# Kernel optimization log

Measured on AMD Instinct MI355X. Metric: run time of the kernel, lower is better.

The kernel has to match this reference:

```python
import jax, jax.numpy as jnp
import numpy as np

WAYS, SHOTS = 5, 5
F_DIM, HID = 1024, 512          # num_node_feats, int(1024*0.5)
BATCH = 2048                    # num_tasks
N = WAYS * SHOTS + 1            # 26 samples per episode
BN_EPS = 1e-5


def setup_inputs() -> dict:
    key = jax.random.key(0)
    ks = jax.random.split(key, 12)
    d = {"node_feats": jax.random.normal(ks[0], (BATCH, N, F_DIM), jnp.float32)}
    # conv1 (1x1): F_DIM -> HID, bn1; conv2: HID -> HID, bn2; conv4: HID -> F_DIM
    d["w1"] = jax.random.normal(ks[1], (HID, F_DIM), jnp.float32) * (1.0 / np.sqrt(F_DIM))
    d["b1"] = jax.random.normal(ks[2], (HID,), jnp.float32) * 0.01
    d["g1"] = jnp.ones((HID,), jnp.float32)
    d["be1"] = jnp.zeros((HID,), jnp.float32)
    d["m1"] = jax.random.normal(ks[3], (HID,), jnp.float32) * 0.1
    d["v1"] = jax.random.uniform(ks[4], (HID,), jnp.float32, 0.5, 1.5)
    d["w2"] = jax.random.normal(ks[5], (HID, HID), jnp.float32) * (1.0 / np.sqrt(HID))
    d["b2"] = jax.random.normal(ks[6], (HID,), jnp.float32) * 0.01
    d["g2"] = jnp.ones((HID,), jnp.float32)
    d["be2"] = jnp.zeros((HID,), jnp.float32)
    d["m2"] = jax.random.normal(ks[7], (HID,), jnp.float32) * 0.1
    d["v2"] = jax.random.uniform(ks[8], (HID,), jnp.float32, 0.5, 1.5)
    d["w3"] = jax.random.normal(ks[9], (F_DIM, HID), jnp.float32) * (1.0 / np.sqrt(HID))
    d["b3"] = jax.random.normal(ks[10], (F_DIM,), jnp.float32) * 0.01
    return d


def _conv1x1(x, w, b):
    # x: [B, Cin, N], w: [Cout, Cin] -> [B, Cout, N]
    return jnp.einsum('bcn,oc->bon', x, w) + b[None, :, None]


def _bn(x, g, be, m, v):
    # inference BatchNorm1d over channel dim of [B, C, N]
    scale = g / jnp.sqrt(v + BN_EPS)
    return (x - m[None, :, None]) * scale[None, :, None] + be[None, :, None]


def _forward(node_feats, w1, b1, g1, be1, m1, v1, w2, b2, g2, be2, m2, v2, w3, b3):
    B, n, F = node_feats.shape  # n == WAYS*SHOTS+1
    # in-place per-class mean on the transpose view also mutates node_feats in torch:
    sup = node_feats[:, :WAYS * SHOTS].reshape(B, WAYS, SHOTS, F)
    sup = jnp.broadcast_to(sup.mean(axis=2, keepdims=True), sup.shape).reshape(B, WAYS * SHOTS, F)
    nf = jnp.concatenate([sup, node_feats[:, WAYS * SHOTS:]], axis=1)  # [B, N, F]

    x = nf.transpose(0, 2, 1)  # [B, F, N]
    x = jax.nn.leaky_relu(_bn(_conv1x1(x, w1, b1), g1, be1, m1, v1), 0.01)
    x = jax.nn.leaky_relu(_bn(_conv1x1(x, w2, b2), g2, be2, m2, v2), 0.01)
    att = jax.nn.sigmoid(_conv1x1(x, w3, b3))  # [B, F, N]

    # sim_cal: cosine sim of u_ij = a_i*a_j*x_i vs v_ij = a_i*a_j*x_j, fused into matmuls.
    a = att.transpose(0, 2, 1)       # [B, N, F]
    a2 = a * a                       # attention squared
    P = a2 * nf                      # dot(u,v)   = (P P^T)[i,j]
    Q = a2 * nf * nf                 # ||u_ij||^2 = (Q a2^T)[i,j]
    dots = jnp.einsum('bif,bjf->bij', P, P)    # [B, N, N]
    n2 = jnp.einsum('bif,bjf->bij', Q, a2)     # [B, N, N]
    nrm = jnp.sqrt(n2)
    sim = dots / (nrm * nrm.transpose(0, 2, 1))
    pred = jnp.stack([sim, 1.0 - sim], axis=1)  # [B, 2, N, N]
    return jnp.clip(pred, 0.0, 1.0)


def reference(node_feats, w1, b1, g1, be1, m1, v1, w2, b2, g2, be2, m2, v2, w3, b3):
    return _forward(node_feats, w1, b1, g1, be1, m1, v1, w2, b2, g2, be2, m2, v2, w3, b3)
```

## Files before the change

### kernel.cpp

```cpp
#include <hip/hip_runtime.h>
#include <hip/hip_bf16.h>
#include <math.h>

typedef __bf16 bf16_t;
typedef bf16_t bf16x8 __attribute__((ext_vector_type(8)));
typedef float f32x4 __attribute__((ext_vector_type(4)));

#define WAYS 5
#define SHOTS 5
#define F_DIM 1024
#define HID 512
#define BATCH 2048
#define NN 26
#define NC 6
#define MROWS (BATCH * NC)

#define S1 (HID * F_DIM)
#define S2 (HID * HID)
#define S3 (F_DIM * HID)

__global__ __launch_bounds__(256)
void cvt_all_kernel(const float* __restrict__ w1, const float* __restrict__ w2,
                    const float* __restrict__ w3, bf16_t* __restrict__ out) {
    int i = (blockIdx.x * 256 + threadIdx.x) * 4;
    if (i >= S1 + S2 + S3) return;
    const float* src;
    int j = i;
    if (i < S1)            { src = w1; }
    else if (i < S1 + S2)  { src = w2; j = i - S1; }
    else                   { src = w3; j = i - S1 - S2; }
    float4 v = *(const float4*)(src + j);
    out[i + 0] = (bf16_t)v.x;
    out[i + 1] = (bf16_t)v.y;
    out[i + 2] = (bf16_t)v.z;
    out[i + 3] = (bf16_t)v.w;
}

__global__ __launch_bounds__(128)
void nfc_kernel(const float* __restrict__ node, bf16_t* __restrict__ nfc_b) {
    int row = blockIdx.x;
    int b = row / NC;
    int w = row - b * NC;
    int f = threadIdx.x * 8;
    const float* src = node + (size_t)b * NN * F_DIM;
    float acc[8];
    if (w < WAYS) {
        #pragma unroll
        for (int e = 0; e < 8; ++e) acc[e] = 0.f;
        #pragma unroll
        for (int s = 0; s < SHOTS; ++s) {
            const float* r = src + (size_t)(w * SHOTS + s) * F_DIM + f;
            float4 v0 = *(const float4*)r;
            float4 v1 = *(const float4*)(r + 4);
            acc[0] += v0.x; acc[1] += v0.y; acc[2] += v0.z; acc[3] += v0.w;
            acc[4] += v1.x; acc[5] += v1.y; acc[6] += v1.z; acc[7] += v1.w;
        }
        #pragma unroll
        for (int e = 0; e < 8; ++e) acc[e] *= 0.2f;
    } else {
        const float* r = src + (size_t)25 * F_DIM + f;
        float4 v0 = *(const float4*)r;
        float4 v1 = *(const float4*)(r + 4);
        acc[0] = v0.x; acc[1] = v0.y; acc[2] = v0.z; acc[3] = v0.w;
        acc[4] = v1.x; acc[5] = v1.y; acc[6] = v1.z; acc[7] = v1.w;
    }
    bf16x8 ob;
    #pragma unroll
    for (int e = 0; e < 8; ++e) ob[e] = (bf16_t)acc[e];
    *(bf16x8*)(nfc_b + (size_t)row * F_DIM + f) = ob;
}

template<int EPI, int TN>
__global__ __launch_bounds__(256)
void gemm_bt(const bf16_t* __restrict__ A, const bf16_t* __restrict__ W,
             bf16_t* __restrict__ C, int M, int N, int K,
             const float* __restrict__ bias, const float* __restrict__ gam,
             const float* __restrict__ bet, const float* __restrict__ mu,
             const float* __restrict__ var) {
    constexpr int NI = TN / 32;
    __shared__ bf16_t As[128 * 32];
    __shared__ bf16_t Bs[TN * 32];
    const int tid = threadIdx.x;
    const int lane = tid & 63, wid = tid >> 6;
    const int bm = blockIdx.y * 128, bn = blockIdx.x * TN;
    const int l15 = lane & 15, quad = lane >> 4;
    const int wm = (wid & 1) * 64, wn = (wid >> 1) * (TN / 2);

    const int srowA = wid * 32;
    const int srowB = wid * (TN / 4);
    const int lrow = lane >> 2;
    const int lcol = (lane & 3) * 8;
    const bf16_t* gA = A + (size_t)(bm + srowA + lrow) * K + lcol;
    const bf16_t* gB = W + (size_t)(bn + srowB + lrow) * K + lcol;
    bf16_t* lA = &As[srowA * 32];
    bf16_t* lB = &Bs[srowB * 32];

    f32x4 acc[4][NI] = {};

    for (int k0 = 0; k0 < K; k0 += 32) {
        __syncthreads();
        #pragma unroll
        for (int q = 0; q < 2; ++q)
            __builtin_amdgcn_global_load_lds(
                (const __attribute__((address_space(1))) void*)(gA + (size_t)q * 16 * K + k0),
                (__attribute__((address_space(3))) void*)(lA + q * 16 * 32), 16, 0, 0);
        #pragma unroll
        for (int q = 0; q < TN / 64; ++q)
            __builtin_amdgcn_global_load_lds(
                (const __attribute__((address_space(1))) void*)(gB + (size_t)q * 16 * K + k0),
                (__attribute__((address_space(3))) void*)(lB + q * 16 * 32), 16, 0, 0);
        __syncthreads();
        bf16x8 af[4], bfr[NI];
        #pragma unroll
        for (int mi = 0; mi < 4; ++mi)
            af[mi] = *(const bf16x8*)&As[(wm + mi * 16 + l15) * 32 + quad * 8];
        #pragma unroll
        for (int ni = 0; ni < NI; ++ni)
            bfr[ni] = *(const bf16x8*)&Bs[(wn + ni * 16 + l15) * 32 + quad * 8];
        #pragma unroll
        for (int mi = 0; mi < 4; ++mi)
            #pragma unroll
            for (int ni = 0; ni < NI; ++ni)
                acc[mi][ni] = __builtin_amdgcn_mfma_f32_16x16x32_bf16(af[mi], bfr[ni], acc[mi][ni], 0, 0, 0);
    }

    #pragma unroll
    for (int ni = 0; ni < NI; ++ni) {
        const int n = bn + wn + ni * 16 + l15;
        float s, t;
        if constexpr (EPI == 0) {
            float sg = gam[n] * rsqrtf(var[n] + 1e-5f);
            s = sg;
            t = (bias[n] - mu[n]) * sg + bet[n];
        } else {
            s = 1.0f;
            t = bias[n];
        }
        #pragma unroll
        for (int mi = 0; mi < 4; ++mi) {
            const int m = bm + wm + mi * 16 + quad * 4;
            #pragma unroll
            for (int r = 0; r < 4; ++r) {
                float y = acc[mi][ni][r] * s + t;
                if constexpr (EPI == 0) {
                    y = y > 0.0f ? y : 0.01f * y;
                } else {
                    y = 1.0f / (1.0f + __expf(-y));
                }
                C[(size_t)(m + r) * N + n] = (bf16_t)y;
            }
        }
    }
}

__global__ __launch_bounds__(256)
void sim_kernel(const bf16_t* __restrict__ nfc, const bf16_t* __restrict__ att,
                float* __restrict__ out) {
    __shared__ float sx[NC * F_DIM];
    __shared__ float sa[NC * F_DIM];
    __shared__ float dmat[NC * NC], n2mat[NC * NC], simc[NC * NC];
    const int b = blockIdx.x, tid = threadIdx.x;
    const bf16_t* xs = nfc + (size_t)b * NC * F_DIM;
    const bf16_t* as = att + (size_t)b * NC * F_DIM;
    for (int i = tid * 8; i < NC * F_DIM; i += 256 * 8) {
        bf16x8 vx = *(const bf16x8*)&xs[i];
        bf16x8 va = *(const bf16x8*)&as[i];
        #pragma unroll
        for (int e = 0; e < 8; ++e) { sx[i + e] = (float)vx[e]; sa[i + e] = (float)va[e]; }
    }
    __syncthreads();
    const int lane = tid & 63, wid = tid >> 6;
    const int ti[21] = {0,0,0,0,0,0,1,1,1,1,1,2,2,2,2,3,3,3,4,4,5};
    const int tj[21] = {0,1,2,3,4,5,1,2,3,4,5,2,3,4,5,3,4,5,4,5,5};
    for (int t = wid; t < 21; t += 4) {
        const int i = ti[t], j = tj[t];
        float d = 0.f, qij = 0.f, qji = 0.f;
        for (int f = lane; f < F_DIM; f += 64) {
            float ai = sa[i * F_DIM + f], aj = sa[j * F_DIM + f];
            float xi = sx[i * F_DIM + f], xj = sx[j * F_DIM + f];
            float a2i = ai * ai, a2j = aj * aj;
            float pi = a2i * xi, pj = a2j * xj;
            d   += pi * pj;
            qij += pi * xi * a2j;
            qji += pj * xj * a2i;
        }
        #pragma unroll
        for (int off = 32; off > 0; off >>= 1) {
            d   += __shfl_xor(d, off);
            qij += __shfl_xor(qij, off);
            qji += __shfl_xor(qji, off);
        }
        if (lane == 0) {
            dmat[i * NC + j] = d; dmat[j * NC + i] = d;
            n2mat[i * NC + j] = qij; n2mat[j * NC + i] = qji;
        }
    }
    __syncthreads();
    if (tid < NC * NC) {
        int i = tid / NC, j = tid - (tid / NC) * NC;
        simc[tid] = dmat[tid] / sqrtf(n2mat[i * NC + j] * n2mat[j * NC + i]);
    }
    __syncthreads();
    float* o = out + (size_t)b * (2 * NN * NN);
    for (int e = tid; e < 2 * NN * NN; e += 256) {
        int ch = e / (NN * NN);
        int rem = e - ch * (NN * NN);
        int i = rem / NN, j = rem - (rem / NN) * NN;
        float s = simc[(i / 5) * NC + (j / 5)];
        float v = ch ? 1.0f - s : s;
        v = fminf(fmaxf(v, 0.0f), 1.0f);
        o[e] = v;
    }
}

extern "C" void kernel_launch(void* const* d_in, const int* in_sizes, int n_in,
                              void* d_out, int out_size, void* d_ws, size_t ws_size,
                              hipStream_t stream) {
    const float* node = (const float*)d_in[0];
    const float* w1  = (const float*)d_in[1];
    const float* b1  = (const float*)d_in[2];
    const float* g1  = (const float*)d_in[3];
    const float* be1 = (const float*)d_in[4];
    const float* m1  = (const float*)d_in[5];
    const float* v1  = (const float*)d_in[6];
    const float* w2  = (const float*)d_in[7];
    const float* b2  = (const float*)d_in[8];
    const float* g2  = (const float*)d_in[9];
    const float* be2 = (const float*)d_in[10];
    const float* m2  = (const float*)d_in[11];
    const float* v2  = (const float*)d_in[12];
    const float* w3  = (const float*)d_in[13];
    const float* b3  = (const float*)d_in[14];
    float* out = (float*)d_out;

    char* ws = (char*)d_ws;
    size_t off = 0;
    bf16_t* wall  = (bf16_t*)(ws + off); off += (size_t)(S1 + S2 + S3) * 2;
    bf16_t* w1b = wall, *w2b = wall + S1, *w3b = wall + S1 + S2;
    bf16_t* nfc_b = (bf16_t*)(ws + off); off += (size_t)MROWS * F_DIM * 2;
    bf16_t* x1    = (bf16_t*)(ws + off); off += (size_t)MROWS * HID * 2;
    bf16_t* x2    = (bf16_t*)(ws + off); off += (size_t)MROWS * HID * 2;
    bf16_t* attb  = (bf16_t*)(ws + off); off += (size_t)MROWS * F_DIM * 2;

    cvt_all_kernel<<<((S1 + S2 + S3) / 4 + 255) / 256, 256, 0, stream>>>(w1, w2, w3, wall);
    nfc_kernel<<<MROWS, 128, 0, stream>>>(node, nfc_b);
    gemm_bt<0, 64><<<dim3(HID / 64, MROWS / 128), 256, 0, stream>>>(
        nfc_b, w1b, x1, MROWS, HID, F_DIM, b1, g1, be1, m1, v1);
    gemm_bt<0, 64><<<dim3(HID / 64, MROWS / 128), 256, 0, stream>>>(
        x1, w2b, x2, MROWS, HID, HID, b2, g2, be2, m2, v2);
    gemm_bt<1, 128><<<dim3(F_DIM / 128, MROWS / 128), 256, 0, stream>>>(
        x2, w3b, attb, MROWS, F_DIM, HID, b3, nullptr, nullptr, nullptr, nullptr);
    sim_kernel<<<BATCH, 256, 0, stream>>>(nfc_b, attb, out);
}
```

Before: 443.9 us.

## Merge prep kernels, double-buffer GEMM LDS, swizzle blocks, stream sim directly

Merges the weight conversion and the support-mean kernels into one launch and vectorises the bf16 stores. The GEMM now double-buffers its LDS tiles so the next k-slice is staged while MFMAs run on the current one, and it remaps block IDs in an XCD-style swizzle to improve L2 locality. The sim kernel drops its LDS staging and reads bf16 vectors straight from global memory with computed pair indices. Together these aim to cut launch overhead, load-latency stalls and LDS traffic, at the cost of more LDS per GEMM block and repeated global reads in the sim kernel.

```diff
diff --git a/kernel.cpp b/kernel.cpp
--- a/kernel.cpp
+++ b/kernel.cpp
@@ -4,6 +4,7 @@
 
 typedef __bf16 bf16_t;
 typedef bf16_t bf16x8 __attribute__((ext_vector_type(8)));
+typedef bf16_t bf16x4 __attribute__((ext_vector_type(4)));
 typedef float f32x4 __attribute__((ext_vector_type(4)));
 
 #define WAYS 5
@@ -18,27 +19,27 @@
 #define S1 (HID * F_DIM)
 #define S2 (HID * HID)
 #define S3 (F_DIM * HID)
-
-__global__ __launch_bounds__(256)
-void cvt_all_kernel(const float* __restrict__ w1, const float* __restrict__ w2,
-                    const float* __restrict__ w3, bf16_t* __restrict__ out) {
-    int i = (blockIdx.x * 256 + threadIdx.x) * 4;
-    if (i >= S1 + S2 + S3) return;
-    const float* src;
-    int j = i;
-    if (i < S1)            { src = w1; }
-    else if (i < S1 + S2)  { src = w2; j = i - S1; }
-    else                   { src = w3; j = i - S1 - S2; }
-    float4 v = *(const float4*)(src + j);
-    out[i + 0] = (bf16_t)v.x;
-    out[i + 1] = (bf16_t)v.y;
-    out[i + 2] = (bf16_t)v.z;
-    out[i + 3] = (bf16_t)v.w;
-}
+#define CVT_BLOCKS ((S1 + S2 + S3) / 512)
 
 __global__ __launch_bounds__(128)
-void nfc_kernel(const float* __restrict__ node, bf16_t* __restrict__ nfc_b) {
-    int row = blockIdx.x;
+void prep_kernel(const float* __restrict__ node,
+                 const float* __restrict__ w1, const float* __restrict__ w2,
+                 const float* __restrict__ w3, bf16_t* __restrict__ wall,
+                 bf16_t* __restrict__ nfc_b) {
+    if (blockIdx.x < CVT_BLOCKS) {
+        int i = (blockIdx.x * 128 + threadIdx.x) * 4;
+        const float* src;
+        int j = i;
+        if (i < S1)            { src = w1; }
+        else if (i < S1 + S2)  { src = w2; j = i - S1; }
+        else                   { src = w3; j = i - S1 - S2; }
+        float4 v = *(const float4*)(src + j);
+        bf16x4 o;
+        o[0] = (bf16_t)v.x; o[1] = (bf16_t)v.y; o[2] = (bf16_t)v.z; o[3] = (bf16_t)v.w;
+        *(bf16x4*)(wall + i) = o;
+        return;
+    }
+    int row = blockIdx.x - CVT_BLOCKS;
     int b = row / NC;
     int w = row - b * NC;
     int f = threadIdx.x * 8;
@@ -78,11 +79,18 @@
              const float* __restrict__ bet, const float* __restrict__ mu,
              const float* __restrict__ var) {
     constexpr int NI = TN / 32;
-    __shared__ bf16_t As[128 * 32];
-    __shared__ bf16_t Bs[TN * 32];
+    __shared__ bf16_t As[2][128 * 32];
+    __shared__ bf16_t Bs[2][TN * 32];
     const int tid = threadIdx.x;
     const int lane = tid & 63, wid = tid >> 6;
-    const int bm = blockIdx.y * 128, bn = blockIdx.x * TN;
+
+    const int nwg = gridDim.x * gridDim.y;
+    const int orig = blockIdx.y * gridDim.x + blockIdx.x;
+    const int wg = (orig & 7) * (nwg >> 3) + (orig >> 3);
+    const int bxi = wg & (gridDim.x - 1);
+    const int byi = wg / gridDim.x;
+    const int bm = byi * 128, bn = bxi * TN;
+
     const int l15 = lane & 15, quad = lane >> 4;
     const int wm = (wid & 1) * 64, wn = (wid >> 1) * (TN / 2);
 
@@ -92,13 +100,12 @@
     const int lcol = (lane & 3) * 8;
     const bf16_t* gA = A + (size_t)(bm + srowA + lrow) * K + lcol;
     const bf16_t* gB = W + (size_t)(bn + srowB + lrow) * K + lcol;
-    bf16_t* lA = &As[srowA * 32];
-    bf16_t* lB = &Bs[srowB * 32];
 
     f32x4 acc[4][NI] = {};
 
-    for (int k0 = 0; k0 < K; k0 += 32) {
-        __syncthreads();
+    auto stage = [&](int buf, int k0) {
+        bf16_t* lA = &As[buf][srowA * 32];
+        bf16_t* lB = &Bs[buf][srowB * 32];
         #pragma unroll
         for (int q = 0; q < 2; ++q)
             __builtin_amdgcn_global_load_lds(
@@ -109,19 +116,27 @@
             __builtin_amdgcn_global_load_lds(
                 (const __attribute__((address_space(1))) void*)(gB + (size_t)q * 16 * K + k0),
                 (__attribute__((address_space(3))) void*)(lB + q * 16 * 32), 16, 0, 0);
-        __syncthreads();
+    };
+
+    stage(0, 0);
+    __syncthreads();
+    int cur = 0;
+    for (int k0 = 0; k0 < K; k0 += 32) {
+        if (k0 + 32 < K) stage(cur ^ 1, k0 + 32);
         bf16x8 af[4], bfr[NI];
         #pragma unroll
         for (int mi = 0; mi < 4; ++mi)
-            af[mi] = *(const bf16x8*)&As[(wm + mi * 16 + l15) * 32 + quad * 8];
+            af[mi] = *(const bf16x8*)&As[cur][(wm + mi * 16 + l15) * 32 + quad * 8];
         #pragma unroll
         for (int ni = 0; ni < NI; ++ni)
-            bfr[ni] = *(const bf16x8*)&Bs[(wn + ni * 16 + l15) * 32 + quad * 8];
+            bfr[ni] = *(const bf16x8*)&Bs[cur][(wn + ni * 16 + l15) * 32 + quad * 8];
         #pragma unroll
         for (int mi = 0; mi < 4; ++mi)
             #pragma unroll
             for (int ni = 0; ni < NI; ++ni)
                 acc[mi][ni] = __builtin_amdgcn_mfma_f32_16x16x32_bf16(af[mi], bfr[ni], acc[mi][ni], 0, 0, 0);
+        __syncthreads();
+        cur ^= 1;
     }
 
     #pragma unroll
@@ -156,33 +171,32 @@
 __global__ __launch_bounds__(256)
 void sim_kernel(const bf16_t* __restrict__ nfc, const bf16_t* __restrict__ att,
                 float* __restrict__ out) {
-    __shared__ float sx[NC * F_DIM];
-    __shared__ float sa[NC * F_DIM];
     __shared__ float dmat[NC * NC], n2mat[NC * NC], simc[NC * NC];
     const int b = blockIdx.x, tid = threadIdx.x;
     const bf16_t* xs = nfc + (size_t)b * NC * F_DIM;
     const bf16_t* as = att + (size_t)b * NC * F_DIM;
-    for (int i = tid * 8; i < NC * F_DIM; i += 256 * 8) {
-        bf16x8 vx = *(const bf16x8*)&xs[i];
-        bf16x8 va = *(const bf16x8*)&as[i];
-        #pragma unroll
-        for (int e = 0; e < 8; ++e) { sx[i + e] = (float)vx[e]; sa[i + e] = (float)va[e]; }
-    }
-    __syncthreads();
     const int lane = tid & 63, wid = tid >> 6;
-    const int ti[21] = {0,0,0,0,0,0,1,1,1,1,1,2,2,2,2,3,3,3,4,4,5};
-    const int tj[21] = {0,1,2,3,4,5,1,2,3,4,5,2,3,4,5,3,4,5,4,5,5};
     for (int t = wid; t < 21; t += 4) {
-        const int i = ti[t], j = tj[t];
+        const int i = (t >= 6) + (t >= 11) + (t >= 15) + (t >= 18) + (t >= 20);
+        const int j = t - (i * (13 - i)) / 2 + i;
         float d = 0.f, qij = 0.f, qji = 0.f;
-        for (int f = lane; f < F_DIM; f += 64) {
-            float ai = sa[i * F_DIM + f], aj = sa[j * F_DIM + f];
-            float xi = sx[i * F_DIM + f], xj = sx[j * F_DIM + f];
-            float a2i = ai * ai, a2j = aj * aj;
-            float pi = a2i * xi, pj = a2j * xj;
-            d   += pi * pj;
-            qij += pi * xi * a2j;
-            qji += pj * xj * a2i;
+        #pragma unroll
+        for (int c = 0; c < 2; ++c) {
+            const int f0 = lane * 8 + c * 512;
+            bf16x8 vai = *(const bf16x8*)&as[i * F_DIM + f0];
+            bf16x8 vaj = *(const bf16x8*)&as[j * F_DIM + f0];
+            bf16x8 vxi = *(const bf16x8*)&xs[i * F_DIM + f0];
+            bf16x8 vxj = *(const bf16x8*)&xs[j * F_DIM + f0];
+            #pragma unroll
+            for (int e = 0; e < 8; ++e) {
+                float ai = (float)vai[e], aj = (float)vaj[e];
+                float xi = (float)vxi[e], xj = (float)vxj[e];
+                float a2i = ai * ai, a2j = aj * aj;
+                float pi = a2i * xi, pj = a2j * xj;
+                d   += pi * pj;
+                qij += pi * xi * a2j;
+                qji += pj * xj * a2i;
+            }
         }
         #pragma unroll
         for (int off = 32; off > 0; off >>= 1) {
@@ -242,8 +256,7 @@
     bf16_t* x2    = (bf16_t*)(ws + off); off += (size_t)MROWS * HID * 2;
     bf16_t* attb  = (bf16_t*)(ws + off); off += (size_t)MROWS * F_DIM * 2;
 
-    cvt_all_kernel<<<((S1 + S2 + S3) / 4 + 255) / 256, 256, 0, stream>>>(w1, w2, w3, wall);
-    nfc_kernel<<<MROWS, 128, 0, stream>>>(node, nfc_b);
+    prep_kernel<<<CVT_BLOCKS + MROWS, 128, 0, stream>>>(node, w1, w2, w3, wall, nfc_b);
     gemm_bt<0, 64><<<dim3(HID / 64, MROWS / 128), 256, 0, stream>>>(
         nfc_b, w1b, x1, MROWS, HID, F_DIM, b1, g1, be1, m1, v1);
     gemm_bt<0, 64><<<dim3(HID / 64, MROWS / 128), 256, 0, stream>>>(
```

Result: faster. 406.8 us, median of 2 (-8.4%).
